# Optimization experiments

Hardware: AMD Instinct MI355X
Metric: run time of the kernel (lower is better)

Reference implementation:

```python
import jax, jax.numpy as jnp
import numpy as np
from jax import lax

STRIDE = 2
PAD = 1
EPS = 1e-6
K = 2  # top-k experts
E = 4  # num_experts
B, C1, H, W = 32, 64, 64, 64
C2 = 128
PATCH = 3


def conv_ln(x, w, b, gamma, beta):
    # Conv2d(c1->c2, patch, stride, pad) followed by channel-first LayerNorm
    y = lax.conv_general_dilated(x, w, (STRIDE, STRIDE), ((PAD, PAD), (PAD, PAD)),
                                 dimension_numbers=('NCHW', 'OIHW', 'NCHW'))
    y = y + b[None, :, None, None]
    u = y.mean(1, keepdims=True)
    s = ((y - u) ** 2).mean(1, keepdims=True)
    y = (y - u) / jnp.sqrt(s + EPS)
    return gamma[None, :, None, None] * y + beta[None, :, None, None]


def setup_inputs() -> dict:
    key = jax.random.key(0)
    ks = jax.random.split(key, 10)
    x = jax.random.normal(ks[0], (B, C1, H, W), dtype=jnp.float32)
    w_gate = jax.random.normal(ks[1], (C1, E), dtype=jnp.float32) * 0.02
    expert_w = jax.random.normal(ks[2], (E, C2, C1, PATCH, PATCH), dtype=jnp.float32) * 0.05
    expert_b = jax.random.normal(ks[3], (E, C2), dtype=jnp.float32) * 0.01
    expert_ln_w = jnp.ones((E, C2), dtype=jnp.float32)
    expert_ln_b = jnp.zeros((E, C2), dtype=jnp.float32)
    shared_w = jax.random.normal(ks[4], (C2, C1, PATCH, PATCH), dtype=jnp.float32) * 0.05
    shared_b = jax.random.normal(ks[5], (C2,), dtype=jnp.float32) * 0.01
    shared_ln_w = jnp.ones((C2,), dtype=jnp.float32)
    shared_ln_b = jnp.zeros((C2,), dtype=jnp.float32)
    return {"x": x, "w_gate": w_gate,
            "expert_w": expert_w, "expert_b": expert_b,
            "expert_ln_w": expert_ln_w, "expert_ln_b": expert_ln_b,
            "shared_w": shared_w, "shared_b": shared_b,
            "shared_ln_w": shared_ln_w, "shared_ln_b": shared_ln_b}


def reference(x, w_gate, expert_w, expert_b, expert_ln_w, expert_ln_b,
              shared_w, shared_b, shared_ln_w, shared_ln_b):
    # --- noisy top-k gating (eval mode: no noise) ---
    gate_in = x.mean(axis=(2, 3))            # [B, width]
    logits = gate_in @ w_gate                # [B, E]
    top_vals, top_idx = lax.top_k(logits, K) # [B, K]
    top_gates = jax.nn.softmax(top_vals, axis=-1)
    # scatter top-k gate values back to dense [B, E] gate matrix
    gates = jnp.sum(jax.nn.one_hot(top_idx, E, dtype=x.dtype) * top_gates[..., None], axis=1)
    # --- per-expert conv+LN; dense-weighted combine is math-equivalent to
    #     SparseDispatcher dispatch -> expert -> weighted index_add combine ---
    expert_out = jax.vmap(lambda w, b, g, bt: conv_ln(x, w, b, g, bt))(
        expert_w, expert_b, expert_ln_w, expert_ln_b)   # [E, B, C2, H', W']
    combined = jnp.einsum('be,ebchw->bchw', gates, expert_out)
    # --- shared expert added to routed output ---
    shared = conv_ln(x, shared_w, shared_b, shared_ln_w, shared_ln_b)
    return combined + shared
```

## Files before the change

kernel.cpp:

```cpp
#include <hip/hip_runtime.h>
#include <cstdint>
#include <cstddef>

#define NB    32
#define NC1   64
#define NC2   128
#define NE    4
#define NSLOT 5
#define HIN   64
#define WIN   64
#define HOUT  32
#define WOUT  32

#define GATEIN_OFF 0
#define BIAS_OFF   2176
#define GAMMA_OFF  2816
#define BETA_OFF   3456
#define WBF_OFF    4096

typedef __bf16 bf16x8 __attribute__((ext_vector_type(8)));
typedef float  f32x16 __attribute__((ext_vector_type(16)));

#define GLOAD_LDS16(G, L)                                                        \
    __builtin_amdgcn_global_load_lds(                                            \
        (const __attribute__((address_space(1))) void*)(G),                      \
        (__attribute__((address_space(3))) void*)(L), 16, 0, 0)

__global__ void prep2_kernel(const float* __restrict__ x,
                             const float* __restrict__ expert_w,
                             const float* __restrict__ shared_w,
                             const float* __restrict__ expert_b,
                             const float* __restrict__ shared_b,
                             const float* __restrict__ eln_w,
                             const float* __restrict__ sln_w,
                             const float* __restrict__ eln_b,
                             const float* __restrict__ sln_b,
                             float* __restrict__ ws) {
    int bid = blockIdx.x;
    if (bid < 1440) {
        int i = bid * 256 + threadIdx.x;
        {
            int j    = i & 7;
            int l    = (i >> 3) & 63;
            int kk   = (i >> 9) & 3;
            int wv   = (i >> 11) & 3;
            int rest = i >> 13;
            int tap  = rest % 9;
            int e    = rest / 9;
            int c2 = wv * 32 + (l & 31);
            int c  = kk * 16 + (l >> 5) * 8 + j;
            float v;
            if (e < NE) v = expert_w[(((size_t)(e * NC2 + c2) * NC1 + c) * 9) + tap];
            else        v = shared_w[(((size_t)c2 * NC1 + c) * 9) + tap];
            ((__bf16*)(ws + WBF_OFF))[i] = (__bf16)v;
        }
        if (i < NSLOT * NC2) {
            int e = i >> 7, c2 = i & 127;
            ws[BIAS_OFF  + i] = (e < NE) ? expert_b[i] : shared_b[c2];
            ws[GAMMA_OFF + i] = (e < NE) ? eln_w[i]    : sln_w[c2];
            ws[BETA_OFF  + i] = (e < NE) ? eln_b[i]    : sln_b[c2];
        }
    } else {
        int row  = (bid - 1440) * 4 + (threadIdx.x >> 6);
        int lane = threadIdx.x & 63;
        const float* src = x + (size_t)row * (HIN * WIN);
        float s = 0.f;
        for (int i = lane * 4; i < HIN * WIN; i += 64 * 4) {
            float4 v = *(const float4*)(src + i);
            s += v.x + v.y + v.z + v.w;
        }
        #pragma unroll
        for (int off = 32; off >= 1; off >>= 1) s += __shfl_xor(s, off);
        if (lane == 0) ws[GATEIN_OFF + row] = s * (1.f / (HIN * WIN));
    }
}

#define XS_IDX(r, p, ps, c7) ((((r) * 65 + (p)) << 6) + ((ps) << 3) + (c7))
#define XS_BYTES   41600
#define WBUF_ELEMS 24576

__global__ __launch_bounds__(512, 2) void fused_kernel(
        const float* __restrict__ x,
        const float* __restrict__ w_gate,
        const float* __restrict__ ws,
        float* __restrict__ out) {
    __shared__ __align__(16) unsigned char smem[XS_BYTES + 2 * 49152 + 6144];
    __bf16* xs  = (__bf16*)smem;
    __bf16* wb  = (__bf16*)(smem + XS_BYTES);
    float*  red = (float*)(smem + XS_BYTES + 2 * 49152);

    const int bid = blockIdx.x;
    const int b   = bid >> 4;
    const int hg  = bid & 15;
    const int tid = threadIdx.x;
    const int ln  = tid & 63;
    const int wv8 = tid >> 6;
    const int tg  = wv8 >> 2;
    const int wv  = wv8 & 3;
    const int cl  = ln & 31;
    const int hl  = ln >> 5;
    const int wbase = wv * 32;

    int s0, s1; float ga, gb;
    {
        float gi = ws[GATEIN_OFF + b * NC1 + ln];
        float l[NE];
        #pragma unroll
        for (int e = 0; e < NE; ++e) {
            float p = gi * w_gate[ln * NE + e];
            #pragma unroll
            for (int off = 32; off >= 1; off >>= 1) p += __shfl_xor(p, off);
            l[e] = p;
        }
        int i0 = 0; float v0 = l[0];
        #pragma unroll
        for (int e = 1; e < NE; ++e) if (l[e] > v0) { v0 = l[e]; i0 = e; }
        int i1 = -1; float v1 = -3.4e38f;
        #pragma unroll
        for (int e = 0; e < NE; ++e) if (e != i0 && l[e] > v1) { v1 = l[e]; i1 = e; }
        float e1 = expf(v1 - v0);
        float denom = 1.f + e1;
        s0 = i0; ga = 1.f / denom;
        s1 = i1; gb = e1 / denom;
    }

    const __bf16* wtab = (const __bf16*)(ws + WBF_OFF);
    #define ISSUE_W(TAP, BUF)                                                     \
    {                                                                             \
        _Pragma("unroll")                                                         \
        for (int i = 0; i < 6; ++i) {                                             \
            int chunk = wv8 * 6 + i;                     \
            int si    = chunk >> 4;                            \
            int off   = (chunk & 15) << 9;               \
            int sl    = (si == 0) ? s0 : ((si == 1) ? s1 : 4);                    \
            const __bf16* g = wtab + (size_t)sl * 73728 + (TAP) * 8192 + off + ln * 8; \
            __bf16* d = wb + (BUF) * WBUF_ELEMS + si * 8192 + off;                \
            GLOAD_LDS16(g, d);                                                    \
        }                                                                         \
    }
    ISSUE_W(0, 0)

    #pragma unroll
    for (int r = 0; r < 5; ++r) {
        const int hin = 4 * hg - 1 + r;
        #pragma unroll
        for (int pass = 0; pass < 2; ++pass) {
            int idx = (pass << 9) + tid;
            int c   = idx >> 4;
            int i4  = idx & 15;
            float4 v = make_float4(0.f, 0.f, 0.f, 0.f);
            if (hin >= 0)
                v = *(const float4*)(x + (((size_t)b * NC1 + c) * HIN + hin) * WIN + i4 * 4);
            #pragma unroll
            for (int k = 0; k < 4; ++k) {
                int p  = i4 * 4 + k + 1;
                int ps = (c >> 3) ^ ((p >> 1) & 7);
                float f = (k == 0) ? v.x : (k == 1) ? v.y : (k == 2) ? v.z : v.w;
                xs[XS_IDX(r, p, ps, c & 7)] = (__bf16)f;
            }
        }
    }
    if (tid < 64) {
        #pragma unroll
        for (int r = 0; r < 5; ++r) xs[XS_IDX(r, 0, (tid >> 3), tid & 7)] = (__bf16)0.f;
    }

    const int rowbase = wbase + 4 * hl;
    f32x16 acc0, acc1, acc2;
    #define INIT_ACC(ACC, SID)                                                  \
    {                                                                           \
        const float4* bp = (const float4*)(ws + BIAS_OFF + (SID) * NC2 + rowbase); \
        float4 b0 = bp[0], b1 = bp[2], b2 = bp[4], b3 = bp[6];                  \
        ACC[0]=b0.x; ACC[1]=b0.y; ACC[2]=b0.z; ACC[3]=b0.w;                     \
        ACC[4]=b1.x; ACC[5]=b1.y; ACC[6]=b1.z; ACC[7]=b1.w;                     \
        ACC[8]=b2.x; ACC[9]=b2.y; ACC[10]=b2.z; ACC[11]=b2.w;                   \
        ACC[12]=b3.x; ACC[13]=b3.y; ACC[14]=b3.z; ACC[15]=b3.w;                 \
    }
    INIT_ACC(acc0, s0) INIT_ACC(acc1, s1) INIT_ACC(acc2, 4)

    __syncthreads();

    #define MFMA(A, B, C) C = __builtin_amdgcn_mfma_f32_32x32x16_bf16(A, B, C, 0, 0, 0)
    const int p_l = 2 * cl;
    #pragma unroll
    for (int t = 0; t < 9; ++t) {
        if (t < 8) { ISSUE_W(t + 1, (t + 1) & 1) }
        const int r3  = t / 3;
        const int kw  = t % 3;
        const int r   = r3 + 2 * tg;
        const int p   = p_l + kw;
        const int swb = (p >> 1) & 7;
        const __bf16* wbc = wb + (t & 1) * WBUF_ELEMS + wv * 2048 + ln * 8;
        #pragma unroll
        for (int kk = 0; kk < 4; ++kk) {
            bf16x8 bb = *(const bf16x8*)&xs[XS_IDX(r, p, (2 * kk + hl) ^ swb, 0)];
            bf16x8 a0 = *(const bf16x8*)(wbc + 0 * 8192 + kk * 512);
            bf16x8 a1 = *(const bf16x8*)(wbc + 1 * 8192 + kk * 512);
            bf16x8 a2 = *(const bf16x8*)(wbc + 2 * 8192 + kk * 512);
            MFMA(a0, bb, acc0);
            MFMA(a1, bb, acc1);
            MFMA(a2, bb, acc2);
        }
        __syncthreads();
    }

    #define PUT_RED(ACC, SI)                                                      \
    {                                                                             \
        float sum = 0.f, sq = 0.f;                                                \
        _Pragma("unroll")                                                         \
        for (int i = 0; i < 16; ++i) { float a = ACC[i]; sum += a; sq += a * a; } \
        sum += __shfl_xor(sum, 32); sq += __shfl_xor(sq, 32);                     \
        if (ln < 32) {                                                            \
            red[(((SI) * 2 + tg) * 2 + 0) * 128 + wbase + cl] = sum;              \
            red[(((SI) * 2 + tg) * 2 + 1) * 128 + wbase + cl] = sq;               \
        }                                                                         \
    }
    PUT_RED(acc0, 0)
    PUT_RED(acc1, 1)
    PUT_RED(acc2, 2)
    __syncthreads();

    float fin[16];
    #pragma unroll
    for (int i = 0; i < 16; ++i) fin[i] = 0.f;

    #define APPLY(ACC, SI, SID, G)                                                \
    {                                                                             \
        float tot = 0.f, totq = 0.f;                                              \
        _Pragma("unroll")                                                         \
        for (int w = 0; w < 4; ++w) {                                             \
            tot  += red[(((SI) * 2 + tg) * 2 + 0) * 128 + w * 32 + cl];           \
            totq += red[(((SI) * 2 + tg) * 2 + 1) * 128 + w * 32 + cl];           \
        }                                                                         \
        float mean = tot * (1.f / NC2);                                           \
        float var  = totq * (1.f / NC2) - mean * mean;                            \
        float rstd = rsqrtf(var + 1e-6f);                                         \
        const float4* gmp = (const float4*)(ws + GAMMA_OFF + (SID) * NC2 + rowbase); \
        const float4* btp = (const float4*)(ws + BETA_OFF  + (SID) * NC2 + rowbase); \
        float4 g0 = gmp[0], g1 = gmp[2], g2 = gmp[4], g3 = gmp[6];                \
        float4 t0 = btp[0], t1 = btp[2], t2 = btp[4], t3 = btp[6];                \
        float gm[16] = {g0.x,g0.y,g0.z,g0.w, g1.x,g1.y,g1.z,g1.w,                 \
                        g2.x,g2.y,g2.z,g2.w, g3.x,g3.y,g3.z,g3.w};                \
        float bt[16] = {t0.x,t0.y,t0.z,t0.w, t1.x,t1.y,t1.z,t1.w,                 \
                        t2.x,t2.y,t2.z,t2.w, t3.x,t3.y,t3.z,t3.w};                \
        _Pragma("unroll")                                                         \
        for (int i = 0; i < 16; ++i) {                                            \
            float nrm = (ACC[i] - mean) * rstd;                                   \
            fin[i] = fmaf((G), fmaf(gm[i], nrm, bt[i]), fin[i]);                  \
        }                                                                         \
    }
    APPLY(acc0, 0, s0, ga)
    APPLY(acc1, 1, s1, gb)
    APPLY(acc2, 2, 4, 1.0f)

    float* ob = (float*)(smem + XS_BYTES);
    #pragma unroll
    for (int i = 0; i < 16; ++i) {
        int c2 = rowbase + (i & 3) + 8 * (i >> 2);
        ob[(tg * 128 + c2) * 32 + cl] = fin[i];
    }
    __syncthreads();
    for (int idx = tid; idx < 2048; idx += 512) {
        int t2  = idx >> 10;
        int rem = idx & 1023;
        int c2  = rem >> 3;
        int q   = rem & 7;
        float4 v = *(const float4*)&ob[(t2 * 128 + c2) * 32 + q * 4];
        *(float4*)(out + (((size_t)b * NC2 + c2) * HOUT + 2 * hg + t2) * WOUT + q * 4) = v;
    }
}

extern "C" void kernel_launch(void* const* d_in, const int* in_sizes, int n_in,
                              void* d_out, int out_size, void* d_ws, size_t ws_size,
                              hipStream_t stream) {
    const float* x        = (const float*)d_in[0];
    const float* w_gate   = (const float*)d_in[1];
    const float* expert_w = (const float*)d_in[2];
    const float* expert_b = (const float*)d_in[3];
    const float* eln_w    = (const float*)d_in[4];
    const float* eln_b    = (const float*)d_in[5];
    const float* shared_w = (const float*)d_in[6];
    const float* shared_b = (const float*)d_in[7];
    const float* sln_w    = (const float*)d_in[8];
    const float* sln_b    = (const float*)d_in[9];
    float* ws  = (float*)d_ws;
    float* out = (float*)d_out;

    prep2_kernel<<<1952, 256, 0, stream>>>(x, expert_w, shared_w, expert_b, shared_b,
                                           eln_w, sln_w, eln_b, sln_b, ws);
    fused_kernel<<<NB * 16, 512, 0, stream>>>(x, w_gate, ws, out);
}
```

Measured before the change: 47.26 us.

## Use 4-wave blocks with per-wave weight ring and barrier-free pipelined MFMA loop

The block shrinks from 8 to 4 waves, and each wave now computes both output rows, so every weight fragment is reused across two MFMAs. Each wave loads its own slice of weights into a private LDS double-buffer ring two taps ahead. Progress is tracked with explicit vmcnt/lgkmcnt waits, which removes the per-tap __syncthreads. The cost is fewer waves per block, lower occupancy (launch bounds 256,1) and twice the accumulator registers.

```diff
diff --git a/kernel.cpp b/kernel.cpp
--- a/kernel.cpp
+++ b/kernel.cpp
@@ -77,26 +77,25 @@
 
 #define XS_IDX(r, p, ps, c7) ((((r) * 65 + (p)) << 6) + ((ps) << 3) + (c7))
 #define XS_BYTES   41600
-#define WBUF_ELEMS 24576
-
-__global__ __launch_bounds__(512, 2) void fused_kernel(
+#define RING_BYTES 98304
+#define RING_WV    12288
+
+__global__ __launch_bounds__(256, 1) void fused_kernel(
         const float* __restrict__ x,
         const float* __restrict__ w_gate,
         const float* __restrict__ ws,
         float* __restrict__ out) {
-    __shared__ __align__(16) unsigned char smem[XS_BYTES + 2 * 49152 + 6144];
-    __bf16* xs  = (__bf16*)smem;
-    __bf16* wb  = (__bf16*)(smem + XS_BYTES);
-    float*  red = (float*)(smem + XS_BYTES + 2 * 49152);
+    __shared__ __align__(16) unsigned char smem[XS_BYTES + RING_BYTES + 6144];
+    __bf16* xs   = (__bf16*)smem;
+    __bf16* ring = (__bf16*)(smem + XS_BYTES);
+    float*  red  = (float*)(smem + XS_BYTES + RING_BYTES);
 
     const int bid = blockIdx.x;
     const int b   = bid >> 4;
     const int hg  = bid & 15;
     const int tid = threadIdx.x;
     const int ln  = tid & 63;
-    const int wv8 = tid >> 6;
-    const int tg  = wv8 >> 2;
-    const int wv  = wv8 & 3;
+    const int wv  = tid >> 6;
     const int cl  = ln & 31;
     const int hl  = ln >> 5;
     const int wbase = wv * 32;
@@ -124,40 +123,21 @@
         s1 = i1; gb = e1 / denom;
     }
 
-    const __bf16* wtab = (const __bf16*)(ws + WBF_OFF);
-    #define ISSUE_W(TAP, BUF)                                                     \
-    {                                                                             \
-        _Pragma("unroll")                                                         \
-        for (int i = 0; i < 6; ++i) {                                             \
-            int chunk = wv8 * 6 + i;                     \
-            int si    = chunk >> 4;                            \
-            int off   = (chunk & 15) << 9;               \
-            int sl    = (si == 0) ? s0 : ((si == 1) ? s1 : 4);                    \
-            const __bf16* g = wtab + (size_t)sl * 73728 + (TAP) * 8192 + off + ln * 8; \
-            __bf16* d = wb + (BUF) * WBUF_ELEMS + si * 8192 + off;                \
-            GLOAD_LDS16(g, d);                                                    \
-        }                                                                         \
-    }
-    ISSUE_W(0, 0)
-
-    #pragma unroll
-    for (int r = 0; r < 5; ++r) {
-        const int hin = 4 * hg - 1 + r;
-        #pragma unroll
-        for (int pass = 0; pass < 2; ++pass) {
-            int idx = (pass << 9) + tid;
-            int c   = idx >> 4;
-            int i4  = idx & 15;
-            float4 v = make_float4(0.f, 0.f, 0.f, 0.f);
-            if (hin >= 0)
-                v = *(const float4*)(x + (((size_t)b * NC1 + c) * HIN + hin) * WIN + i4 * 4);
-            #pragma unroll
-            for (int k = 0; k < 4; ++k) {
-                int p  = i4 * 4 + k + 1;
-                int ps = (c >> 3) ^ ((p >> 1) & 7);
-                float f = (k == 0) ? v.x : (k == 1) ? v.y : (k == 2) ? v.z : v.w;
-                xs[XS_IDX(r, p, ps, c & 7)] = (__bf16)f;
-            }
+    for (int idx = tid; idx < 5 * 1024; idx += 256) {
+        int r   = idx >> 10;
+        int rem = idx & 1023;
+        int c   = rem >> 4;
+        int i4  = rem & 15;
+        int hin = 4 * hg - 1 + r;
+        float4 v = make_float4(0.f, 0.f, 0.f, 0.f);
+        if (hin >= 0)
+            v = *(const float4*)(x + (((size_t)b * NC1 + c) * HIN + hin) * WIN + i4 * 4);
+        #pragma unroll
+        for (int k = 0; k < 4; ++k) {
+            int p  = i4 * 4 + k + 1;
+            int ps = (c >> 3) ^ ((p >> 1) & 7);
+            float f = (k == 0) ? v.x : (k == 1) ? v.y : (k == 2) ? v.z : v.w;
+            xs[XS_IDX(r, p, ps, c & 7)] = (__bf16)f;
         }
     }
     if (tid < 64) {
@@ -166,7 +146,7 @@
     }
 
     const int rowbase = wbase + 4 * hl;
-    f32x16 acc0, acc1, acc2;
+    f32x16 a00, a01, a10, a11, a20, a21;
     #define INIT_ACC(ACC, SID)                                                  \
     {                                                                           \
         const float4* bp = (const float4*)(ws + BIAS_OFF + (SID) * NC2 + rowbase); \
@@ -176,91 +156,142 @@
         ACC[8]=b2.x; ACC[9]=b2.y; ACC[10]=b2.z; ACC[11]=b2.w;                   \
         ACC[12]=b3.x; ACC[13]=b3.y; ACC[14]=b3.z; ACC[15]=b3.w;                 \
     }
-    INIT_ACC(acc0, s0) INIT_ACC(acc1, s1) INIT_ACC(acc2, 4)
+    INIT_ACC(a00, s0) a01 = a00;
+    INIT_ACC(a10, s1) a11 = a10;
+    INIT_ACC(a20, 4)  a21 = a20;
 
     __syncthreads();
+
+    const __bf16* wtab = (const __bf16*)(ws + WBF_OFF);
+    #define ISSUE_W(TAP, BUF)                                                     \
+    {                                                                             \
+        _Pragma("unroll")                                                         \
+        for (int ch = 0; ch < 12; ++ch) {                                         \
+            int si = ch >> 2, kk = ch & 3;                                        \
+            int sl = (si == 0) ? s0 : ((si == 1) ? s1 : 4);                       \
+            const __bf16* g = wtab + (size_t)sl * 73728 + (TAP) * 8192            \
+                              + wv * 2048 + kk * 512 + ln * 8;                    \
+            __bf16* d = ring + wv * RING_WV + (BUF) * 6144 + ch * 512;            \
+            GLOAD_LDS16(g, d);                                                    \
+        }                                                                         \
+    }
+    ISSUE_W(0, 0)
+    ISSUE_W(1, 1)
 
     #define MFMA(A, B, C) C = __builtin_amdgcn_mfma_f32_32x32x16_bf16(A, B, C, 0, 0, 0)
     const int p_l = 2 * cl;
     #pragma unroll
     for (int t = 0; t < 9; ++t) {
-        if (t < 8) { ISSUE_W(t + 1, (t + 1) & 1) }
+        if (t < 8) { asm volatile("s_waitcnt vmcnt(12)" ::: "memory"); }
+        else       { asm volatile("s_waitcnt vmcnt(0)"  ::: "memory"); }
+
         const int r3  = t / 3;
         const int kw  = t % 3;
-        const int r   = r3 + 2 * tg;
         const int p   = p_l + kw;
         const int swb = (p >> 1) & 7;
-        const __bf16* wbc = wb + (t & 1) * WBUF_ELEMS + wv * 2048 + ln * 8;
-        #pragma unroll
-        for (int kk = 0; kk < 4; ++kk) {
-            bf16x8 bb = *(const bf16x8*)&xs[XS_IDX(r, p, (2 * kk + hl) ^ swb, 0)];
-            bf16x8 a0 = *(const bf16x8*)(wbc + 0 * 8192 + kk * 512);
-            bf16x8 a1 = *(const bf16x8*)(wbc + 1 * 8192 + kk * 512);
-            bf16x8 a2 = *(const bf16x8*)(wbc + 2 * 8192 + kk * 512);
-            MFMA(a0, bb, acc0);
-            MFMA(a1, bb, acc1);
-            MFMA(a2, bb, acc2);
-        }
-        __syncthreads();
-    }
-
-    #define PUT_RED(ACC, SI)                                                      \
+        const __bf16* rb = ring + wv * RING_WV + (t & 1) * 6144 + ln * 8;
+
+        bf16x8 bA0 = *(const bf16x8*)&xs[XS_IDX(r3,     p, (0 + hl) ^ swb, 0)];
+        bf16x8 bA1 = *(const bf16x8*)&xs[XS_IDX(r3,     p, (2 + hl) ^ swb, 0)];
+        bf16x8 bA2 = *(const bf16x8*)&xs[XS_IDX(r3,     p, (4 + hl) ^ swb, 0)];
+        bf16x8 bA3 = *(const bf16x8*)&xs[XS_IDX(r3,     p, (6 + hl) ^ swb, 0)];
+        bf16x8 bB0 = *(const bf16x8*)&xs[XS_IDX(r3 + 2, p, (0 + hl) ^ swb, 0)];
+        bf16x8 bB1 = *(const bf16x8*)&xs[XS_IDX(r3 + 2, p, (2 + hl) ^ swb, 0)];
+        bf16x8 bB2 = *(const bf16x8*)&xs[XS_IDX(r3 + 2, p, (4 + hl) ^ swb, 0)];
+        bf16x8 bB3 = *(const bf16x8*)&xs[XS_IDX(r3 + 2, p, (6 + hl) ^ swb, 0)];
+
+        bf16x8 v;
+        v = *(const bf16x8*)(rb + 0  * 512); MFMA(v, bA0, a00); MFMA(v, bB0, a01);
+        v = *(const bf16x8*)(rb + 1  * 512); MFMA(v, bA1, a00); MFMA(v, bB1, a01);
+        v = *(const bf16x8*)(rb + 2  * 512); MFMA(v, bA2, a00); MFMA(v, bB2, a01);
+        v = *(const bf16x8*)(rb + 3  * 512); MFMA(v, bA3, a00); MFMA(v, bB3, a01);
+        v = *(const bf16x8*)(rb + 4  * 512); MFMA(v, bA0, a10); MFMA(v, bB0, a11);
+        v = *(const bf16x8*)(rb + 5  * 512); MFMA(v, bA1, a10); MFMA(v, bB1, a11);
+        v = *(const bf16x8*)(rb + 6  * 512); MFMA(v, bA2, a10); MFMA(v, bB2, a11);
+        v = *(const bf16x8*)(rb + 7  * 512); MFMA(v, bA3, a10); MFMA(v, bB3, a11);
+        v = *(const bf16x8*)(rb + 8  * 512); MFMA(v, bA0, a20); MFMA(v, bB0, a21);
+        v = *(const bf16x8*)(rb + 9  * 512); MFMA(v, bA1, a20); MFMA(v, bB1, a21);
+        v = *(const bf16x8*)(rb + 10 * 512); MFMA(v, bA2, a20); MFMA(v, bB2, a21);
+        v = *(const bf16x8*)(rb + 11 * 512); MFMA(v, bA3, a20); MFMA(v, bB3, a21);
+
+        asm volatile("s_waitcnt lgkmcnt(0)" ::: "memory");
+        if (t < 7) { ISSUE_W(t + 2, (t & 1)) }
+    }
+
+    #define PUT_RED(ACC, SI, TG)                                                  \
     {                                                                             \
         float sum = 0.f, sq = 0.f;                                                \
         _Pragma("unroll")                                                         \
         for (int i = 0; i < 16; ++i) { float a = ACC[i]; sum += a; sq += a * a; } \
         sum += __shfl_xor(sum, 32); sq += __shfl_xor(sq, 32);                     \
         if (ln < 32) {                                                            \
-            red[(((SI) * 2 + tg) * 2 + 0) * 128 + wbase + cl] = sum;              \
-            red[(((SI) * 2 + tg) * 2 + 1) * 128 + wbase + cl] = sq;               \
+            red[(((SI) * 2 + (TG)) * 2 + 0) * 128 + wbase + cl] = sum;            \
+            red[(((SI) * 2 + (TG)) * 2 + 1) * 128 + wbase + cl] = sq;             \
         }                                                                         \
     }
-    PUT_RED(acc0, 0)
-    PUT_RED(acc1, 1)
-    PUT_RED(acc2, 2)
+    PUT_RED(a00, 0, 0) PUT_RED(a01, 0, 1)
+    PUT_RED(a10, 1, 0) PUT_RED(a11, 1, 1)
+    PUT_RED(a20, 2, 0) PUT_RED(a21, 2, 1)
     __syncthreads();
 
-    float fin[16];
+    float fin0[16], fin1[16];
     #pragma unroll
-    for (int i = 0; i < 16; ++i) fin[i] = 0.f;
-
-    #define APPLY(ACC, SI, SID, G)                                                \
+    for (int i = 0; i < 16; ++i) { fin0[i] = 0.f; fin1[i] = 0.f; }
+
+    #define APPLY(ACC, FIN, SI, TG, GM, BT, G)                                    \
     {                                                                             \
         float tot = 0.f, totq = 0.f;                                              \
         _Pragma("unroll")                                                         \
         for (int w = 0; w < 4; ++w) {                                             \
-            tot  += red[(((SI) * 2 + tg) * 2 + 0) * 128 + w * 32 + cl];           \
-            totq += red[(((SI) * 2 + tg) * 2 + 1) * 128 + w * 32 + cl];           \
+            tot  += red[(((SI) * 2 + (TG)) * 2 + 0) * 128 + w * 32 + cl];         \
+            totq += red[(((SI) * 2 + (TG)) * 2 + 1) * 128 + w * 32 + cl];         \
         }                                                                         \
         float mean = tot * (1.f / NC2);                                           \
         float var  = totq * (1.f / NC2) - mean * mean;                            \
         float rstd = rsqrtf(var + 1e-6f);                                         \
-        const float4* gmp = (const float4*)(ws + GAMMA_OFF + (SID) * NC2 + rowbase); \
-        const float4* btp = (const float4*)(ws + BETA_OFF  + (SID) * NC2 + rowbase); \
-        float4 g0 = gmp[0], g1 = gmp[2], g2 = gmp[4], g3 = gmp[6];                \
-        float4 t0 = btp[0], t1 = btp[2], t2 = btp[4], t3 = btp[6];                \
-        float gm[16] = {g0.x,g0.y,g0.z,g0.w, g1.x,g1.y,g1.z,g1.w,                 \
-                        g2.x,g2.y,g2.z,g2.w, g3.x,g3.y,g3.z,g3.w};                \
-        float bt[16] = {t0.x,t0.y,t0.z,t0.w, t1.x,t1.y,t1.z,t1.w,                 \
-                        t2.x,t2.y,t2.z,t2.w, t3.x,t3.y,t3.z,t3.w};                \
         _Pragma("unroll")                                                         \
         for (int i = 0; i < 16; ++i) {                                            \
             float nrm = (ACC[i] - mean) * rstd;                                   \
-            fin[i] = fmaf((G), fmaf(gm[i], nrm, bt[i]), fin[i]);                  \
+            FIN[i] = fmaf((G), fmaf(GM[i], nrm, BT[i]), FIN[i]);                  \
         }                                                                         \
     }
-    APPLY(acc0, 0, s0, ga)
-    APPLY(acc1, 1, s1, gb)
-    APPLY(acc2, 2, 4, 1.0f)
+    #define LOAD_GB(SID, GM, BT)                                                  \
+        float GM[16], BT[16];                                                     \
+        {                                                                         \
+            const float4* gmp = (const float4*)(ws + GAMMA_OFF + (SID) * NC2 + rowbase); \
+            const float4* btp = (const float4*)(ws + BETA_OFF  + (SID) * NC2 + rowbase); \
+            float4 g0 = gmp[0], g1 = gmp[2], g2 = gmp[4], g3 = gmp[6];            \
+            float4 t0 = btp[0], t1 = btp[2], t2 = btp[4], t3 = btp[6];            \
+            GM[0]=g0.x;GM[1]=g0.y;GM[2]=g0.z;GM[3]=g0.w;GM[4]=g1.x;GM[5]=g1.y;GM[6]=g1.z;GM[7]=g1.w; \
+            GM[8]=g2.x;GM[9]=g2.y;GM[10]=g2.z;GM[11]=g2.w;GM[12]=g3.x;GM[13]=g3.y;GM[14]=g3.z;GM[15]=g3.w; \
+            BT[0]=t0.x;BT[1]=t0.y;BT[2]=t0.z;BT[3]=t0.w;BT[4]=t1.x;BT[5]=t1.y;BT[6]=t1.z;BT[7]=t1.w; \
+            BT[8]=t2.x;BT[9]=t2.y;BT[10]=t2.z;BT[11]=t2.w;BT[12]=t3.x;BT[13]=t3.y;BT[14]=t3.z;BT[15]=t3.w; \
+        }
+    {
+        LOAD_GB(s0, gm0, bt0)
+        APPLY(a00, fin0, 0, 0, gm0, bt0, ga)
+        APPLY(a01, fin1, 0, 1, gm0, bt0, ga)
+    }
+    {
+        LOAD_GB(s1, gm1, bt1)
+        APPLY(a10, fin0, 1, 0, gm1, bt1, gb)
+        APPLY(a11, fin1, 1, 1, gm1, bt1, gb)
+    }
+    {
+        LOAD_GB(4, gm2, bt2)
+        APPLY(a20, fin0, 2, 0, gm2, bt2, 1.0f)
+        APPLY(a21, fin1, 2, 1, gm2, bt2, 1.0f)
+    }
 
     float* ob = (float*)(smem + XS_BYTES);
     #pragma unroll
     for (int i = 0; i < 16; ++i) {
         int c2 = rowbase + (i & 3) + 8 * (i >> 2);
-        ob[(tg * 128 + c2) * 32 + cl] = fin[i];
+        ob[(0 * 128 + c2) * 32 + cl] = fin0[i];
+        ob[(1 * 128 + c2) * 32 + cl] = fin1[i];
     }
     __syncthreads();
-    for (int idx = tid; idx < 2048; idx += 512) {
+    for (int idx = tid; idx < 2048; idx += 256) {
         int t2  = idx >> 10;
         int rem = idx & 1023;
         int c2  = rem >> 3;
@@ -288,5 +319,5 @@
 
     prep2_kernel<<<1952, 256, 0, stream>>>(x, expert_w, shared_w, expert_b, shared_b,
                                            eln_w, sln_w, eln_b, sln_b, ws);
-    fused_kernel<<<NB * 16, 512, 0, stream>>>(x, w_gate, ws, out);
+    fused_kernel<<<NB * 16, 256, 0, stream>>>(x, w_gate, ws, out);
 }
```

After: 56.73 us. +20.0%, slower.
